# Kernel optimization log

Hardware: AMD Instinct MI355X
Metric: run time of the kernel (lower is better)

Reference implementation:

```python
import jax, jax.numpy as jnp
import numpy as np

H = 4  # num_heads
LN_EPS = 1e-5


def setup_inputs() -> dict:
    key = jax.random.key(0)
    ks = jax.random.split(key, 6)
    B, N, IN, OUT = 4, 2048, 256, 256
    return {
        "node_feats": jax.random.normal(ks[0], (B, N, IN), dtype=jnp.float32),
        "adj_matrix": jax.random.uniform(ks[1], (B, N, N), dtype=jnp.float32),
        "W_lin": jax.random.normal(ks[2], (IN, OUT), dtype=jnp.float32) * (IN ** -0.5),
        "b_lin": jnp.zeros((OUT,), dtype=jnp.float32),
        "W_q": jax.random.normal(ks[3], (IN, OUT), dtype=jnp.float32) * (IN ** -0.5),
        "W_k": jax.random.normal(ks[4], (IN, OUT), dtype=jnp.float32) * (IN ** -0.5),
        "ln_g": jnp.ones((OUT,), dtype=jnp.float32),
        "ln_b": jnp.zeros((OUT,), dtype=jnp.float32),
    }


def _heads(x, B, N):
    # [B,N,OUT] -> [B,H,N,hd]
    return x.reshape(B, N, H, -1).transpose(0, 2, 1, 3)


def reference(node_feats, adj_matrix, W_lin, b_lin, W_q, W_k, ln_g, ln_b):
    B, N, _ = node_feats.shape
    out_dim = W_lin.shape[1]
    hd = out_dim // H
    scale = hd ** -0.5
    lrelu = lambda z: jax.nn.leaky_relu(z, 0.01)

    X = _heads(lrelu(node_feats @ W_lin + b_lin), B, N)   # [B,H,N,hd]
    q = _heads(lrelu(node_feats @ W_q), B, N)
    k = _heads(lrelu(node_feats @ W_k), B, N)

    att = jax.nn.sigmoid(jnp.einsum('bhxd,bhyd->bhxy', q, k) * scale)
    adj_h = adj_matrix[:, None] * att                     # [B,H,N,N]

    # symmetric degree normalization: D^-1/2 A D^-1/2 (broadcast form of diag_embed matmuls)
    deg = jnp.sum(adj_h, axis=-1)                         # [B,H,N]
    dis = jnp.where(deg > 0, deg ** -0.5, 0.0)
    A = dis[..., :, None] * adj_h * dis[..., None, :]

    Y = jnp.einsum('bhxy,bhyd->bhxd', A, X)
    Y = Y.transpose(0, 2, 1, 3).reshape(B, N, out_dim)

    mu = jnp.mean(Y, axis=-1, keepdims=True)
    var = jnp.mean((Y - mu) ** 2, axis=-1, keepdims=True)
    return (Y - mu) * jax.lax.rsqrt(var + LN_EPS) * ln_g + ln_b
```

## Files before the change

### kernel.cpp

```cpp
#include <hip/hip_runtime.h>
#include <hip/hip_bf16.h>

#define B_   4
#define N_   2048
#define IN_  256
#define OUT_ 256
#define H_   4
#define HD_  64
#define LN_EPS 1e-5f

typedef __bf16 bf16x8 __attribute__((ext_vector_type(8)));
typedef float  f32x4  __attribute__((ext_vector_type(4)));
typedef unsigned short u16x8 __attribute__((ext_vector_type(8)));
typedef unsigned int   u32x4 __attribute__((ext_vector_type(4)));

__device__ __forceinline__ unsigned short f2bf(float x) {
    unsigned int u = __float_as_uint(x);
    return (unsigned short)((u + 0x7FFFu + ((u >> 16) & 1u)) >> 16);
}
__device__ __forceinline__ float bf2f(unsigned short u) {
    return __uint_as_float((unsigned int)u << 16);
}
__device__ __forceinline__ unsigned int cvtpk(float lo, float hi) {
    unsigned int r;
    asm("v_cvt_pk_bf16_f32 %0, %1, %2" : "=v"(r) : "v"(lo), "v"(hi));
    return r;
}

__global__ __launch_bounds__(256) void conv_kernel(
    const float* __restrict__ nf, const float* __restrict__ Wl,
    const float* __restrict__ Wq, const float* __restrict__ Wk,
    unsigned short* __restrict__ nfb, unsigned short* __restrict__ Wt)
{
    const int bid = blockIdx.x, tid = threadIdx.x;
    if (bid < 1024) {
        size_t i = ((size_t)bid * 256 + tid) * 8;
        u16x8 o;
        #pragma unroll
        for (int j = 0; j < 8; j++) o[j] = f2bf(nf[i + j]);
        *(u16x8*)&nfb[i] = o;
    } else {
        int t = (bid - 1024) * 256 + tid;
        int z = t >> 16;
        int l = t & 65535;
        int k = l & 255, n = l >> 8;
        const float* W = (z == 0) ? Wl : (z == 1 ? Wq : Wk);
        Wt[(size_t)z * 65536 + n * 256 + k] = f2bf(W[k * 256 + n]);
    }
}

__global__ __launch_bounds__(256) void gemm3_kernel(
    const unsigned short* __restrict__ nfb, const unsigned short* __restrict__ Wt3,
    const float* __restrict__ bl,
    unsigned short* __restrict__ qb, unsigned short* __restrict__ kb,
    unsigned short* __restrict__ Xt)
{
    const int z  = blockIdx.z;
    const int m0 = blockIdx.x * 64, n0 = blockIdx.y * 64;
    const int tid = threadIdx.x, wave = tid >> 6, lane = tid & 63;
    const int lq = lane >> 4, lr = lane & 15;
    const unsigned short* Wt = Wt3 + (size_t)z * 65536;

    f32x4 acc[4] = {};
    #pragma unroll 4
    for (int k0 = 0; k0 < IN_; k0 += 32) {
        bf16x8 af = *(const bf16x8*)&nfb[(size_t)(m0 + wave * 16 + lr) * IN_ + k0 + lq * 8];
        #pragma unroll
        for (int f = 0; f < 4; f++) {
            bf16x8 bfr = *(const bf16x8*)&Wt[(size_t)(n0 + f * 16 + lr) * IN_ + k0 + lq * 8];
            acc[f] = __builtin_amdgcn_mfma_f32_16x16x32_bf16(af, bfr, acc[f], 0, 0, 0);
        }
    }

    #pragma unroll
    for (int f = 0; f < 4; f++) {
        int c = n0 + f * 16 + lr;
        float bias = (z == 0) ? bl[c] : 0.0f;
        #pragma unroll
        for (int r = 0; r < 4; r++) {
            int m = m0 + wave * 16 + lq * 4 + r;
            float v = acc[f][r] + bias;
            v = (v >= 0.f) ? v : 0.01f * v;
            unsigned short bv = f2bf(v);
            if (z == 0) {
                int n = m & (N_ - 1);
                int h = c >> 6, d = c & 63;
                Xt[(((size_t)(m >> 11) * H_ + h) * HD_ + d) * N_ + n] = bv;
            } else {
                unsigned short* dst = (z == 1) ? qb : kb;
                dst[(size_t)m * OUT_ + c] = bv;
            }
        }
    }
}

__global__ __launch_bounds__(256) void att_kernel(
    const float* __restrict__ adj,
    const unsigned short* __restrict__ qb,
    const unsigned short* __restrict__ kb,
    unsigned short* __restrict__ W,
    float* __restrict__ degp,
    int b_base, int SH)
{
    const int s  = blockIdx.z;
    const int bg = b_base + (s >> 2);
    const int hg = s & 3;
    const int x0 = blockIdx.x * 128, y0 = blockIdx.y * 128;
    const int tid = threadIdx.x, wave = tid >> 6, lane = tid & 63;
    const int lq = lane >> 4, lr = lane & 15;
    const int wq = wave >> 1, wn = wave & 1;
    const int wx0 = x0 + wq * 64, wy0 = y0 + wn * 64;
    const float sc = -0.125f * 1.44269504088896f;

    const unsigned short* qrow = qb + (size_t)(bg * N_ + wx0) * OUT_ + hg * HD_;
    const unsigned short* krow = kb + (size_t)(bg * N_ + wy0) * OUT_ + hg * HD_;

    f32x4 acc[4][4] = {};
    #pragma unroll
    for (int ks = 0; ks < 2; ks++) {
        bf16x8 af[4], bf[4];
        #pragma unroll
        for (int mf = 0; mf < 4; mf++)
            af[mf] = *(const bf16x8*)&qrow[(size_t)(mf * 16 + lr) * OUT_ + ks * 32 + lq * 8];
        #pragma unroll
        for (int nf = 0; nf < 4; nf++)
            bf[nf] = *(const bf16x8*)&krow[(size_t)(nf * 16 + lr) * OUT_ + ks * 32 + lq * 8];
        #pragma unroll
        for (int mf = 0; mf < 4; mf++)
            #pragma unroll
            for (int nf = 0; nf < 4; nf++)
                acc[mf][nf] = __builtin_amdgcn_mfma_f32_16x16x32_bf16(af[mf], bf[nf], acc[mf][nf], 0, 0, 0);
    }

    unsigned short* Wp = W + (size_t)s * N_ * N_;
    #pragma unroll
    for (int mf = 0; mf < 4; mf++) {
        #pragma unroll
        for (int r = 0; r < 4; r++) {
            int x = wx0 + mf * 16 + lq * 4 + r;
            const float* arow = adj + ((size_t)bg * N_ + x) * N_ + wy0;
            unsigned short* wrow = Wp + (size_t)x * N_ + wy0;
            float sum = 0.f;
            #pragma unroll
            for (int nf = 0; nf < 4; nf++) {
                float a = arow[nf * 16 + lr];
                float att = __builtin_amdgcn_rcpf(1.f + exp2f(acc[mf][nf][r] * sc));
                float wv = a * att;
                sum += wv;
                wrow[nf * 16 + lr] = f2bf(wv);
            }
            sum += __shfl_xor(sum, 1); sum += __shfl_xor(sum, 2);
            sum += __shfl_xor(sum, 4); sum += __shfl_xor(sum, 8);
            if (lr == 0)
                degp[((size_t)(blockIdx.y * 2 + wn) * SH + s) * N_ + x] = sum;
        }
    }
}

__global__ __launch_bounds__(256) void degsum_kernel(
    const float* __restrict__ degp, float* __restrict__ dis, int b_base, int SH)
{
    int t = blockIdx.x * 256 + threadIdx.x;
    int s = t >> 11, x = t & (N_ - 1);
    float sum = 0.f;
    #pragma unroll
    for (int j = 0; j < 32; j++) sum += degp[((size_t)j * SH + s) * N_ + x];
    dis[((size_t)b_base * H_ + s) * N_ + x] = (sum > 0.f) ? rsqrtf(sum) : 0.f;
}

__global__ __launch_bounds__(256) void scale_kernel(
    const unsigned short* __restrict__ Xt, const float* __restrict__ dis,
    unsigned short* __restrict__ Xs)
{
    int t = blockIdx.x * 256 + threadIdx.x;
    size_t idx = (size_t)t * 8;
    int s = t >> 14;
    int y = (int)(idx & (N_ - 1));
    f32x4 d0 = *(const f32x4*)&dis[(size_t)s * N_ + y];
    f32x4 d1 = *(const f32x4*)&dis[(size_t)s * N_ + y + 4];
    u16x8 x = *(const u16x8*)&Xt[idx];
    u32x4 o;
    o[0] = cvtpk(bf2f(x[0]) * d0[0], bf2f(x[1]) * d0[1]);
    o[1] = cvtpk(bf2f(x[2]) * d0[2], bf2f(x[3]) * d0[3]);
    o[2] = cvtpk(bf2f(x[4]) * d1[0], bf2f(x[5]) * d1[1]);
    o[3] = cvtpk(bf2f(x[6]) * d1[2], bf2f(x[7]) * d1[3]);
    *(u32x4*)&Xs[idx] = o;
}

__global__ __launch_bounds__(256) void yout_kernel(
    const unsigned short* __restrict__ W,
    const unsigned short* __restrict__ Xs,
    const float* __restrict__ dis,
    const float* __restrict__ lng, const float* __restrict__ lnb,
    float* __restrict__ out, int b_base)
{
    const int x0 = blockIdx.x * 16;
    const int bl = blockIdx.y;
    const int bg = b_base + bl;
    const int tid = threadIdx.x, h = tid >> 6, lane = tid & 63;
    const int lq = lane >> 4, lr = lane & 15;
    const int s = bl * H_ + h;

    const unsigned short* Wp = W + (size_t)s * N_ * N_ + (size_t)(x0 + lr) * N_;
    const unsigned short* Xp = Xs + ((size_t)s * HD_ + lr) * N_;

    f32x4 Y[4] = {};
    for (int k0 = 0; k0 < N_; k0 += 64) {
        #pragma unroll
        for (int ks = 0; ks < 2; ks++) {
            bf16x8 af = *(const bf16x8*)&Wp[k0 + ks * 32 + lq * 8];
            #pragma unroll
            for (int db = 0; db < 4; db++) {
                bf16x8 xf = *(const bf16x8*)&Xp[(size_t)db * 16 * N_ + k0 + ks * 32 + lq * 8];
                Y[db] = __builtin_amdgcn_mfma_f32_16x16x32_bf16(af, xf, Y[db], 0, 0, 0);
            }
        }
    }

    float dx[4];
    #pragma unroll
    for (int r = 0; r < 4; r++)
        dx[r] = dis[((size_t)bg * H_ + h) * N_ + x0 + lq * 4 + r];

    __shared__ float lnred[2][4][16];
    float s1[4] = {}, s2[4] = {};
    #pragma unroll
    for (int r = 0; r < 4; r++) {
        #pragma unroll
        for (int db = 0; db < 4; db++) {
            float v = Y[db][r] * dx[r];
            s1[r] += v; s2[r] += v * v;
        }
    }
    #pragma unroll
    for (int r = 0; r < 4; r++) {
        float a = s1[r], q2 = s2[r];
        a += __shfl_xor(a, 1); a += __shfl_xor(a, 2); a += __shfl_xor(a, 4); a += __shfl_xor(a, 8);
        q2 += __shfl_xor(q2, 1); q2 += __shfl_xor(q2, 2); q2 += __shfl_xor(q2, 4); q2 += __shfl_xor(q2, 8);
        s1[r] = a; s2[r] = q2;
    }
    if (lr == 0) {
        #pragma unroll
        for (int r = 0; r < 4; r++) {
            lnred[0][h][lq * 4 + r] = s1[r];
            lnred[1][h][lq * 4 + r] = s2[r];
        }
    }
    __syncthreads();

    float gg[4], bb[4];
    #pragma unroll
    for (int db = 0; db < 4; db++) {
        int c = h * HD_ + db * 16 + lr;
        gg[db] = lng[c]; bb[db] = lnb[c];
    }
    #pragma unroll
    for (int r = 0; r < 4; r++) {
        int xr = lq * 4 + r;
        float t1 = lnred[0][0][xr] + lnred[0][1][xr] + lnred[0][2][xr] + lnred[0][3][xr];
        float t2 = lnred[1][0][xr] + lnred[1][1][xr] + lnred[1][2][xr] + lnred[1][3][xr];
        float mu  = t1 * (1.f / 256.f);
        float var = t2 * (1.f / 256.f) - mu * mu;
        float rs  = rsqrtf(var + LN_EPS);
        #pragma unroll
        for (int db = 0; db < 4; db++) {
            int c = h * HD_ + db * 16 + lr;
            float v = (Y[db][r] * dx[r] - mu) * rs * gg[db] + bb[db];
            out[((size_t)(bg * N_ + x0 + xr)) * OUT_ + c] = v;
        }
    }
}

extern "C" void kernel_launch(void* const* d_in, const int* in_sizes, int n_in,
                              void* d_out, int out_size, void* d_ws, size_t ws_size,
                              hipStream_t stream) {
    const float* nf  = (const float*)d_in[0];
    const float* adj = (const float*)d_in[1];
    const float* Wl  = (const float*)d_in[2];
    const float* bl  = (const float*)d_in[3];
    const float* Wq  = (const float*)d_in[4];
    const float* Wk  = (const float*)d_in[5];
    const float* lng = (const float*)d_in[6];
    const float* lnb = (const float*)d_in[7];
    float* out = (float*)d_out;

    char* w = (char*)d_ws;
    unsigned short* nfb = (unsigned short*)w;  w += (size_t)B_ * N_ * IN_ * 2;
    unsigned short* Wt  = (unsigned short*)w;  w += (size_t)3 * IN_ * OUT_ * 2;
    unsigned short* qb  = (unsigned short*)w;  w += (size_t)B_ * N_ * OUT_ * 2;
    unsigned short* kb  = (unsigned short*)w;  w += (size_t)B_ * N_ * OUT_ * 2;
    unsigned short* Xt  = (unsigned short*)w;  w += (size_t)B_ * N_ * OUT_ * 2;
    unsigned short* Xs  = (unsigned short*)w;  w += (size_t)B_ * N_ * OUT_ * 2;
    float* dis = (float*)w;                    w += (size_t)B_ * H_ * N_ * 4;
    size_t fixed = (size_t)(w - (char*)d_ws);

    size_t need4 = fixed + (size_t)32 * 16 * N_ * 4 + (size_t)16 * N_ * N_ * 2;
    int nb = (ws_size >= need4) ? 4 : 1;
    int SH = nb * H_;
    float* degp = (float*)w;                   w += (size_t)32 * SH * N_ * 4;
    unsigned short* Wbuf = (unsigned short*)w;

    conv_kernel <<<1792, 256, 0, stream>>>(nf, Wl, Wq, Wk, nfb, Wt);
    gemm3_kernel<<<dim3(128, 4, 3), 256, 0, stream>>>(nfb, Wt, bl, qb, kb, Xt);

    for (int b0 = 0; b0 < B_; b0 += nb) {
        size_t xoff = (size_t)b0 * H_ * HD_ * N_;
        att_kernel   <<<dim3(16, 16, SH), 256, 0, stream>>>(adj, qb, kb, Wbuf, degp, b0, SH);
        degsum_kernel<<<SH * N_ / 256, 256, 0, stream>>>(degp, dis, b0, SH);
        scale_kernel <<<SH * HD_ * N_ / 8 / 256, 256, 0, stream>>>(Xt + xoff, dis + (size_t)b0 * H_ * N_, Xs + xoff);
        yout_kernel  <<<dim3(N_ / 16, nb), 256, 0, stream>>>(Wbuf, Xs + xoff, dis, lng, lnb, out, b0);
    }
}
```

Measured before the change: 315.3 us.

## Stage adjacency tile in LDS for coalesced loads/stores; split yout waves across head dims

New measurement: 351.2 us. 11.4% more time.

```diff
diff --git a/kernel.cpp b/kernel.cpp
--- a/kernel.cpp
+++ b/kernel.cpp
@@ -12,6 +12,7 @@
 typedef __bf16 bf16x8 __attribute__((ext_vector_type(8)));
 typedef float  f32x4  __attribute__((ext_vector_type(4)));
 typedef unsigned short u16x8 __attribute__((ext_vector_type(8)));
+typedef unsigned int   u32x2 __attribute__((ext_vector_type(2)));
 typedef unsigned int   u32x4 __attribute__((ext_vector_type(4)));
 
 __device__ __forceinline__ unsigned short f2bf(float x) {
@@ -94,7 +95,7 @@
     }
 }
 
-__global__ __launch_bounds__(256) void att_kernel(
+__global__ __launch_bounds__(256, 4) void att_kernel(
     const float* __restrict__ adj,
     const unsigned short* __restrict__ qb,
     const unsigned short* __restrict__ kb,
@@ -109,51 +110,73 @@
     const int tid = threadIdx.x, wave = tid >> 6, lane = tid & 63;
     const int lq = lane >> 4, lr = lane & 15;
     const int wq = wave >> 1, wn = wave & 1;
-    const int wx0 = x0 + wq * 64, wy0 = y0 + wn * 64;
+    const int wx0 = wq * 64, wy0 = wn * 64;
     const float sc = -0.125f * 1.44269504088896f;
 
-    const unsigned short* qrow = qb + (size_t)(bg * N_ + wx0) * OUT_ + hg * HD_;
-    const unsigned short* krow = kb + (size_t)(bg * N_ + wy0) * OUT_ + hg * HD_;
-
+    __shared__ unsigned short ads[128][136];
+
+    {
+        const int row0 = tid >> 5;
+        const int col  = (tid & 31) * 4;
+        const float* ap = adj + ((size_t)bg * N_ + x0 + row0) * N_ + y0 + col;
+        #pragma unroll 4
+        for (int i = 0; i < 16; i++) {
+            f32x4 v = *(const f32x4*)(ap + (size_t)i * 8 * N_);
+            u32x2 p = { cvtpk(v[0], v[1]), cvtpk(v[2], v[3]) };
+            *(u32x2*)&ads[row0 + i * 8][col] = p;
+        }
+    }
+
+    const unsigned short* qrow = qb + (size_t)(bg * N_ + x0 + wx0) * OUT_ + hg * HD_;
+    const unsigned short* krow = kb + (size_t)(bg * N_ + y0 + wy0) * OUT_ + hg * HD_;
     f32x4 acc[4][4] = {};
     #pragma unroll
     for (int ks = 0; ks < 2; ks++) {
-        bf16x8 af[4], bf[4];
+        bf16x8 af[4];
         #pragma unroll
         for (int mf = 0; mf < 4; mf++)
             af[mf] = *(const bf16x8*)&qrow[(size_t)(mf * 16 + lr) * OUT_ + ks * 32 + lq * 8];
         #pragma unroll
-        for (int nf = 0; nf < 4; nf++)
-            bf[nf] = *(const bf16x8*)&krow[(size_t)(nf * 16 + lr) * OUT_ + ks * 32 + lq * 8];
-        #pragma unroll
-        for (int mf = 0; mf < 4; mf++)
+        for (int nf = 0; nf < 4; nf++) {
+            bf16x8 bfr = *(const bf16x8*)&krow[(size_t)(nf * 16 + lr) * OUT_ + ks * 32 + lq * 8];
             #pragma unroll
-            for (int nf = 0; nf < 4; nf++)
-                acc[mf][nf] = __builtin_amdgcn_mfma_f32_16x16x32_bf16(af[mf], bf[nf], acc[mf][nf], 0, 0, 0);
-    }
-
-    unsigned short* Wp = W + (size_t)s * N_ * N_;
+            for (int mf = 0; mf < 4; mf++)
+                acc[mf][nf] = __builtin_amdgcn_mfma_f32_16x16x32_bf16(af[mf], bfr, acc[mf][nf], 0, 0, 0);
+        }
+    }
+    __syncthreads();
+
     #pragma unroll
     for (int mf = 0; mf < 4; mf++) {
         #pragma unroll
         for (int r = 0; r < 4; r++) {
-            int x = wx0 + mf * 16 + lq * 4 + r;
-            const float* arow = adj + ((size_t)bg * N_ + x) * N_ + wy0;
-            unsigned short* wrow = Wp + (size_t)x * N_ + wy0;
+            const int xl = wx0 + mf * 16 + lq * 4 + r;
             float sum = 0.f;
             #pragma unroll
             for (int nf = 0; nf < 4; nf++) {
-                float a = arow[nf * 16 + lr];
+                const int yl = wy0 + nf * 16 + lr;
+                float a = bf2f(ads[xl][yl]);
                 float att = __builtin_amdgcn_rcpf(1.f + exp2f(acc[mf][nf][r] * sc));
                 float wv = a * att;
+                ads[xl][yl] = (unsigned short)cvtpk(wv, wv);
                 sum += wv;
-                wrow[nf * 16 + lr] = f2bf(wv);
             }
             sum += __shfl_xor(sum, 1); sum += __shfl_xor(sum, 2);
             sum += __shfl_xor(sum, 4); sum += __shfl_xor(sum, 8);
             if (lr == 0)
-                degp[((size_t)(blockIdx.y * 2 + wn) * SH + s) * N_ + x] = sum;
-        }
+                degp[((size_t)(blockIdx.y * 2 + wn) * SH + s) * N_ + x0 + xl] = sum;
+        }
+    }
+    __syncthreads();
+
+    unsigned short* Wp = W + (size_t)s * N_ * N_;
+    const int col = (tid & 15) * 8;
+    const int r0  = tid >> 4;
+    #pragma unroll
+    for (int i = 0; i < 8; i++) {
+        int row = i * 16 + r0;
+        u16x8 v = *(const u16x8*)&ads[row][col];
+        *(u16x8*)&Wp[(size_t)(x0 + row) * N_ + y0 + col] = v;
     }
 }
 
@@ -187,7 +210,7 @@
     *(u32x4*)&Xs[idx] = o;
 }
 
-__global__ __launch_bounds__(256) void yout_kernel(
+__global__ __launch_bounds__(1024, 8) void yout_kernel(
     const unsigned short* __restrict__ W,
     const unsigned short* __restrict__ Xs,
     const float* __restrict__ dis,
@@ -197,23 +220,22 @@
     const int x0 = blockIdx.x * 16;
     const int bl = blockIdx.y;
     const int bg = b_base + bl;
-    const int tid = threadIdx.x, h = tid >> 6, lane = tid & 63;
+    const int tid = threadIdx.x;
+    const int wave = tid >> 6, lane = tid & 63;
+    const int h = wave >> 2, dq = wave & 3;
     const int lq = lane >> 4, lr = lane & 15;
     const int s = bl * H_ + h;
 
     const unsigned short* Wp = W + (size_t)s * N_ * N_ + (size_t)(x0 + lr) * N_;
-    const unsigned short* Xp = Xs + ((size_t)s * HD_ + lr) * N_;
-
-    f32x4 Y[4] = {};
-    for (int k0 = 0; k0 < N_; k0 += 64) {
-        #pragma unroll
-        for (int ks = 0; ks < 2; ks++) {
-            bf16x8 af = *(const bf16x8*)&Wp[k0 + ks * 32 + lq * 8];
-            #pragma unroll
-            for (int db = 0; db < 4; db++) {
-                bf16x8 xf = *(const bf16x8*)&Xp[(size_t)db * 16 * N_ + k0 + ks * 32 + lq * 8];
-                Y[db] = __builtin_amdgcn_mfma_f32_16x16x32_bf16(af, xf, Y[db], 0, 0, 0);
-            }
+    const unsigned short* Xp = Xs + ((size_t)s * HD_ + dq * 16 + lr) * N_;
+
+    f32x4 Y = {};
+    for (int k0 = 0; k0 < N_; k0 += 128) {
+        #pragma unroll
+        for (int u = 0; u < 4; u++) {
+            bf16x8 af = *(const bf16x8*)&Wp[k0 + u * 32 + lq * 8];
+            bf16x8 xf = *(const bf16x8*)&Xp[k0 + u * 32 + lq * 8];
+            Y = __builtin_amdgcn_mfma_f32_16x16x32_bf16(af, xf, Y, 0, 0, 0);
         }
     }
 
@@ -222,52 +244,33 @@
     for (int r = 0; r < 4; r++)
         dx[r] = dis[((size_t)bg * H_ + h) * N_ + x0 + lq * 4 + r];
 
-    __shared__ float lnred[2][4][16];
-    float s1[4] = {}, s2[4] = {};
+    __shared__ float lnred[2][16][16];
+    float v[4];
     #pragma unroll
     for (int r = 0; r < 4; r++) {
-        #pragma unroll
-        for (int db = 0; db < 4; db++) {
-            float v = Y[db][r] * dx[r];
-            s1[r] += v; s2[r] += v * v;
-        }
-    }
-    #pragma unroll
-    for (int r = 0; r < 4; r++) {
-        float a = s1[r], q2 = s2[r];
+        v[r] = Y[r] * dx[r];
+        float a = v[r], q2 = v[r] * v[r];
         a += __shfl_xor(a, 1); a += __shfl_xor(a, 2); a += __shfl_xor(a, 4); a += __shfl_xor(a, 8);
         q2 += __shfl_xor(q2, 1); q2 += __shfl_xor(q2, 2); q2 += __shfl_xor(q2, 4); q2 += __shfl_xor(q2, 8);
-        s1[r] = a; s2[r] = q2;
-    }
-    if (lr == 0) {
-        #pragma unroll
-        for (int r = 0; r < 4; r++) {
-            lnred[0][h][lq * 4 + r] = s1[r];
-            lnred[1][h][lq * 4 + r] = s2[r];
+        if (lr == 0) {
+            lnred[0][wave][lq * 4 + r] = a;
+            lnred[1][wave][lq * 4 + r] = q2;
         }
     }
     __syncthreads();
 
-    float gg[4], bb[4];
-    #pragma unroll
-    for (int db = 0; db < 4; db++) {
-        int c = h * HD_ + db * 16 + lr;
-        gg[db] = lng[c]; bb[db] = lnb[c];
-    }
+    const int c = h * HD_ + dq * 16 + lr;
+    const float g = lng[c], bb = lnb[c];
     #pragma unroll
     for (int r = 0; r < 4; r++) {
-        int xr = lq * 4 + r;
-        float t1 = lnred[0][0][xr] + lnred[0][1][xr] + lnred[0][2][xr] + lnred[0][3][xr];
-        float t2 = lnred[1][0][xr] + lnred[1][1][xr] + lnred[1][2][xr] + lnred[1][3][xr];
+        const int xr = lq * 4 + r;
+        float t1 = 0.f, t2 = 0.f;
+        #pragma unroll
+        for (int wv = 0; wv < 16; wv++) { t1 += lnred[0][wv][xr]; t2 += lnred[1][wv][xr]; }
         float mu  = t1 * (1.f / 256.f);
         float var = t2 * (1.f / 256.f) - mu * mu;
         float rs  = rsqrtf(var + LN_EPS);
-        #pragma unroll
-        for (int db = 0; db < 4; db++) {
-            int c = h * HD_ + db * 16 + lr;
-            float v = (Y[db][r] * dx[r] - mu) * rs * gg[db] + bb[db];
-            out[((size_t)(bg * N_ + x0 + xr)) * OUT_ + c] = v;
-        }
+        out[((size_t)(bg * N_ + x0 + xr)) * OUT_ + c] = (v[r] - mu) * rs * g + bb;
     }
 }
 
@@ -308,6 +311,6 @@
         att_kernel   <<<dim3(16, 16, SH), 256, 0, stream>>>(adj, qb, kb, Wbuf, degp, b0, SH);
         degsum_kernel<<<SH * N_ / 256, 256, 0, stream>>>(degp, dis, b0, SH);
         scale_kernel <<<SH * HD_ * N_ / 8 / 256, 256, 0, stream>>>(Xt + xoff, dis + (size_t)b0 * H_ * N_, Xs + xoff);
-        yout_kernel  <<<dim3(N_ / 16, nb), 256, 0, stream>>>(Wbuf, Xs + xoff, dis, lng, lnb, out, b0);
-    }
-}
+        yout_kernel  <<<dim3(N_ / 16, nb), 1024, 0, stream>>>(Wbuf, Xs + xoff, dis, lng, lnb, out, b0);
+    }
+}
```

## Restructure attention-output GEMM with LDS double-buffered W tiles and separate LayerNorm

Applied to the files above, without the earlier changes.

New measurement: 312.8 us. About the same (-0.8%).

```diff
diff --git a/kernel.cpp b/kernel.cpp
--- a/kernel.cpp
+++ b/kernel.cpp
@@ -187,88 +187,105 @@
     *(u32x4*)&Xs[idx] = o;
 }
 
-__global__ __launch_bounds__(256) void yout_kernel(
+__global__ __launch_bounds__(512) void yout_kernel(
     const unsigned short* __restrict__ W,
     const unsigned short* __restrict__ Xs,
     const float* __restrict__ dis,
+    float* __restrict__ Yraw,
+    int b_base)
+{
+    const int s  = blockIdx.y;
+    const int bg = b_base + (s >> 2);
+    const int hg = s & 3;
+    const int x0 = blockIdx.x * 32;
+    const int tid = threadIdx.x;
+    const int wave = tid >> 6, lane = tid & 63;
+    const int xw = wave >> 2, dq = wave & 3;
+    const int lq = lane >> 4, lr = lane & 15;
+
+    __shared__ unsigned short As[2][32 * 256];
+
+    const int srow = tid >> 4, kslot = tid & 15;
+    const int swz  = (srow & 7) << 4;
+    const unsigned short* Wrow =
+        W + (size_t)s * N_ * N_ + (size_t)(x0 + srow) * N_ + kslot * 16;
+
+    const unsigned short* Xp = Xs + ((size_t)s * HD_ + dq * 16 + lr) * N_;
+
+    const int arow = xw * 16 + lr;
+    const int arsw = (arow & 7) << 4;
+
+    f32x4 Y = {};
+
+    {
+        u16x8 r0 = *(const u16x8*)&Wrow[0];
+        u16x8 r1 = *(const u16x8*)&Wrow[8];
+        char* base = (char*)&As[0][0] + srow * 512;
+        *(u16x8*)(base + ((kslot * 32) ^ swz))      = r0;
+        *(u16x8*)(base + ((kslot * 32 + 16) ^ swz)) = r1;
+    }
+    __syncthreads();
+
+    int cur = 0;
+    for (int kt = 0; kt < 8; kt++) {
+        u16x8 n0, n1;
+        if (kt < 7) {
+            n0 = *(const u16x8*)&Wrow[(kt + 1) * 256];
+            n1 = *(const u16x8*)&Wrow[(kt + 1) * 256 + 8];
+        }
+        const char* abase = (const char*)&As[cur][0] + arow * 512;
+        #pragma unroll
+        for (int half = 0; half < 2; half++) {
+            bf16x8 xf[4];
+            #pragma unroll
+            for (int u = 0; u < 4; u++)
+                xf[u] = *(const bf16x8*)&Xp[kt * 256 + (half * 4 + u) * 32 + lq * 8];
+            #pragma unroll
+            for (int u = 0; u < 4; u++) {
+                const int kb = ((half * 4 + u) * 32 + lq * 8) * 2;
+                bf16x8 af = *(const bf16x8*)(abase + (kb ^ arsw));
+                Y = __builtin_amdgcn_mfma_f32_16x16x32_bf16(af, xf[u], Y, 0, 0, 0);
+            }
+        }
+        if (kt < 7) {
+            char* base = (char*)&As[cur ^ 1][0] + srow * 512;
+            *(u16x8*)(base + ((kslot * 32) ^ swz))      = n0;
+            *(u16x8*)(base + ((kslot * 32 + 16) ^ swz)) = n1;
+        }
+        __syncthreads();
+        cur ^= 1;
+    }
+
+    #pragma unroll
+    for (int r = 0; r < 4; r++) {
+        int x = x0 + xw * 16 + lq * 4 + r;
+        float dx = dis[((size_t)bg * H_ + hg) * N_ + x];
+        Yraw[((size_t)(bg * N_ + x)) * OUT_ + hg * HD_ + dq * 16 + lr] = Y[r] * dx;
+    }
+}
+
+__global__ __launch_bounds__(256) void ln_kernel(
+    const float* __restrict__ Yraw,
     const float* __restrict__ lng, const float* __restrict__ lnb,
-    float* __restrict__ out, int b_base)
-{
-    const int x0 = blockIdx.x * 16;
-    const int bl = blockIdx.y;
-    const int bg = b_base + bl;
-    const int tid = threadIdx.x, h = tid >> 6, lane = tid & 63;
-    const int lq = lane >> 4, lr = lane & 15;
-    const int s = bl * H_ + h;
-
-    const unsigned short* Wp = W + (size_t)s * N_ * N_ + (size_t)(x0 + lr) * N_;
-    const unsigned short* Xp = Xs + ((size_t)s * HD_ + lr) * N_;
-
-    f32x4 Y[4] = {};
-    for (int k0 = 0; k0 < N_; k0 += 64) {
-        #pragma unroll
-        for (int ks = 0; ks < 2; ks++) {
-            bf16x8 af = *(const bf16x8*)&Wp[k0 + ks * 32 + lq * 8];
-            #pragma unroll
-            for (int db = 0; db < 4; db++) {
-                bf16x8 xf = *(const bf16x8*)&Xp[(size_t)db * 16 * N_ + k0 + ks * 32 + lq * 8];
-                Y[db] = __builtin_amdgcn_mfma_f32_16x16x32_bf16(af, xf, Y[db], 0, 0, 0);
-            }
-        }
-    }
-
-    float dx[4];
-    #pragma unroll
-    for (int r = 0; r < 4; r++)
-        dx[r] = dis[((size_t)bg * H_ + h) * N_ + x0 + lq * 4 + r];
-
-    __shared__ float lnred[2][4][16];
-    float s1[4] = {}, s2[4] = {};
-    #pragma unroll
-    for (int r = 0; r < 4; r++) {
-        #pragma unroll
-        for (int db = 0; db < 4; db++) {
-            float v = Y[db][r] * dx[r];
-            s1[r] += v; s2[r] += v * v;
-        }
-    }
-    #pragma unroll
-    for (int r = 0; r < 4; r++) {
-        float a = s1[r], q2 = s2[r];
-        a += __shfl_xor(a, 1); a += __shfl_xor(a, 2); a += __shfl_xor(a, 4); a += __shfl_xor(a, 8);
-        q2 += __shfl_xor(q2, 1); q2 += __shfl_xor(q2, 2); q2 += __shfl_xor(q2, 4); q2 += __shfl_xor(q2, 8);
-        s1[r] = a; s2[r] = q2;
-    }
-    if (lr == 0) {
-        #pragma unroll
-        for (int r = 0; r < 4; r++) {
-            lnred[0][h][lq * 4 + r] = s1[r];
-            lnred[1][h][lq * 4 + r] = s2[r];
-        }
-    }
+    float* __restrict__ out)
+{
+    const int row = blockIdx.x;
+    const int c = threadIdx.x;
+    const size_t base = (size_t)row * OUT_ + c;
+    float v = Yraw[base];
+
+    float s1 = v, s2 = v * v;
+    #pragma unroll
+    for (int d = 1; d < 64; d <<= 1) { s1 += __shfl_xor(s1, d); s2 += __shfl_xor(s2, d); }
+    __shared__ float red[2][4];
+    if ((c & 63) == 0) { red[0][c >> 6] = s1; red[1][c >> 6] = s2; }
     __syncthreads();
-
-    float gg[4], bb[4];
-    #pragma unroll
-    for (int db = 0; db < 4; db++) {
-        int c = h * HD_ + db * 16 + lr;
-        gg[db] = lng[c]; bb[db] = lnb[c];
-    }
-    #pragma unroll
-    for (int r = 0; r < 4; r++) {
-        int xr = lq * 4 + r;
-        float t1 = lnred[0][0][xr] + lnred[0][1][xr] + lnred[0][2][xr] + lnred[0][3][xr];
-        float t2 = lnred[1][0][xr] + lnred[1][1][xr] + lnred[1][2][xr] + lnred[1][3][xr];
-        float mu  = t1 * (1.f / 256.f);
-        float var = t2 * (1.f / 256.f) - mu * mu;
-        float rs  = rsqrtf(var + LN_EPS);
-        #pragma unroll
-        for (int db = 0; db < 4; db++) {
-            int c = h * HD_ + db * 16 + lr;
-            float v = (Y[db][r] * dx[r] - mu) * rs * gg[db] + bb[db];
-            out[((size_t)(bg * N_ + x0 + xr)) * OUT_ + c] = v;
-        }
-    }
+    float t1 = red[0][0] + red[0][1] + red[0][2] + red[0][3];
+    float t2 = red[1][0] + red[1][1] + red[1][2] + red[1][3];
+    float mu  = t1 * (1.f / 256.f);
+    float var = t2 * (1.f / 256.f) - mu * mu;
+    float rs  = rsqrtf(var + LN_EPS);
+    out[base] = (v - mu) * rs * lng[c] + lnb[c];
 }
 
 extern "C" void kernel_launch(void* const* d_in, const int* in_sizes, int n_in,
@@ -291,7 +308,8 @@
     unsigned short* kb  = (unsigned short*)w;  w += (size_t)B_ * N_ * OUT_ * 2;
     unsigned short* Xt  = (unsigned short*)w;  w += (size_t)B_ * N_ * OUT_ * 2;
     unsigned short* Xs  = (unsigned short*)w;  w += (size_t)B_ * N_ * OUT_ * 2;
-    float* dis = (float*)w;                    w += (size_t)B_ * H_ * N_ * 4;
+    float* dis  = (float*)w;                   w += (size_t)B_ * H_ * N_ * 4;
+    float* Yraw = (float*)w;                   w += (size_t)B_ * N_ * OUT_ * 4;
     size_t fixed = (size_t)(w - (char*)d_ws);
 
     size_t need4 = fixed + (size_t)32 * 16 * N_ * 4 + (size_t)16 * N_ * N_ * 2;
@@ -308,6 +326,7 @@
         att_kernel   <<<dim3(16, 16, SH), 256, 0, stream>>>(adj, qb, kb, Wbuf, degp, b0, SH);
         degsum_kernel<<<SH * N_ / 256, 256, 0, stream>>>(degp, dis, b0, SH);
         scale_kernel <<<SH * HD_ * N_ / 8 / 256, 256, 0, stream>>>(Xt + xoff, dis + (size_t)b0 * H_ * N_, Xs + xoff);
-        yout_kernel  <<<dim3(N_ / 16, nb), 256, 0, stream>>>(Wbuf, Xs + xoff, dis, lng, lnb, out, b0);
-    }
-}
+        yout_kernel  <<<dim3(N_ / 32, SH), 512, 0, stream>>>(Wbuf, Xs + xoff, dis, Yraw, b0);
+    }
+    ln_kernel<<<B_ * N_, 256, 0, stream>>>(Yraw, lng, lnb, out);
+}
```
